# Kernel tuning notes

Measured on AMD Instinct MI355X. Metric: run time of the kernel, lower is better.

Reference implementation:

```python
import jax, jax.numpy as jnp
import numpy as np

B, N, D = 4, 2048, 1024
H, S, C, NSH, MV = 8, 3, 32, 3, 4


def _lin(key, fan_in, fan_out):
    k1, k2 = jax.random.split(key)
    lim = 1.0 / np.sqrt(fan_in)
    W = jax.random.uniform(k1, (fan_in, fan_out), minval=-lim, maxval=lim)
    b = jax.random.uniform(k2, (fan_out,), minval=-lim, maxval=lim)
    return W, b


def setup_inputs() -> dict:
    key = jax.random.key(0)
    ks = jax.random.split(key, 16)
    x = jax.random.normal(ks[0], (B, N, D), dtype=jnp.float32)
    W_sense, b_sense = _lin(ks[1], D, S * D)
    W_ctx, b_ctx = _lin(ks[2], D, D)
    W_sel, b_sel = _lin(ks[3], 2 * D, S)
    W_charge, b_charge = _lin(ks[4], D, 1)
    W_shell, b_shell = _lin(ks[5], D, NSH)
    W_class, b_class = _lin(ks[6], D, C)
    W_mass, b_mass = _lin(ks[7], D, 1)
    W_val, b_val = _lin(ks[8], D, MV)
    sparsity = 0.4
    init_val = -np.log(1.0 / sparsity - 1.0)
    compat_logits = jax.random.normal(ks[9], (C, C)) * 0.5 + init_val
    W_v, b_v = _lin(ks[10], D, D)
    W_out, b_out = _lin(ks[11], D, D)
    return {
        'x': x,
        'W_sense': W_sense, 'b_sense': b_sense,
        'W_ctx': W_ctx, 'b_ctx': b_ctx,
        'W_sel': W_sel, 'b_sel': b_sel,
        'W_charge': W_charge, 'b_charge': b_charge,
        'W_shell': W_shell, 'b_shell': b_shell,
        'W_class': W_class, 'b_class': b_class,
        'W_mass': W_mass, 'b_mass': b_mass,
        'W_val': W_val, 'b_val': b_val,
        'compat_logits': compat_logits.astype(jnp.float32),
        'w_charge': jnp.float32(1.0), 'w_shell': jnp.float32(0.5),
        'w_distance': jnp.float32(1.0), 'w_mass': jnp.float32(0.3),
        'w_valence': jnp.float32(0.3), 'temperature': jnp.float32(1.0),
        'W_v': W_v, 'b_v': b_v,
        'W_out': W_out, 'b_out': b_out,
    }


def reference(x, W_sense, b_sense, W_ctx, b_ctx, W_sel, b_sel,
              W_charge, b_charge, W_shell, b_shell, W_class, b_class,
              W_mass, b_mass, W_val, b_val, compat_logits,
              w_charge, w_shell, w_distance, w_mass, w_valence, temperature,
              W_v, b_v, W_out, b_out):
    b, n, d = x.shape
    sp = jax.nn.softplus

    # --- isotope selection (word-sense mixing) ---
    senses = (x @ W_sense + b_sense).reshape(b, n, S, d)          # (B,N,S,D)
    ctx_avg = (x @ W_ctx + b_ctx).mean(axis=1, keepdims=True)     # (B,1,D)
    sel_in = jnp.concatenate([x, jnp.broadcast_to(ctx_avg, (b, n, d))], axis=-1)
    sense_w = jax.nn.softmax(sel_in @ W_sel + b_sel, axis=-1)     # (B,N,S)
    x = jnp.einsum('bns,bnsd->bnd', sense_w, senses)

    # --- atomic properties ---
    charge = jnp.tanh(x @ W_charge + b_charge)[..., 0]            # (B,N)
    shell = jax.nn.softmax(x @ W_shell + b_shell, axis=-1)        # (B,N,NSH)
    cls = jnp.argmax(x @ W_class + b_class, axis=-1)              # (B,N) int
    mass = sp(x @ W_mass + b_mass)[..., 0] + 0.5                  # (B,N)
    val = jax.nn.softmax(x @ W_val + b_val, axis=-1)              # (B,N,MV)

    # --- class compatibility mask (B,N,N) ---
    compat = jax.nn.sigmoid((compat_logits + compat_logits.T) * 0.5)
    sparse_mask = compat[cls[:, :, None], cls[:, None, :]]

    # --- pairwise physics energy (B,N,N) ---
    pos = jnp.arange(n, dtype=x.dtype)
    dist = jnp.abs(pos[:, None] - pos[None, :])                   # (N,N)
    val_sum = val.sum(axis=-1)                                    # (B,N)
    E = (sp(w_charge) * charge[:, :, None] * charge[:, None, :]
         + sp(w_shell) * jnp.abs(shell[:, :, None, :] - shell[:, None, :, :]).sum(-1)
         - sp(w_distance) / (1.0 + 0.1 * dist)
         + sp(w_mass) * 0.1 * mass[:, :, None] * mass[:, None, :]
         - sp(w_valence) * (val_sum[:, :, None] + val_sum[:, None, :]) * 0.5)

    temp = sp(temperature)
    scores = (-E / temp) * sparse_mask
    causal = jnp.triu(jnp.ones((n, n), dtype=bool), k=1)
    scores = jnp.where(causal[None], -jnp.inf, scores)
    attn = jax.nn.softmax(scores, axis=-1)                        # (B,N,N)

    # --- weighted value aggregation (shared attn across heads) ---
    V = (x @ W_v + b_v).reshape(b, n, H, d // H)
    out = jnp.einsum('bij,bjhd->bihd', attn, V).reshape(b, n, d)
    return out @ W_out + b_out
```

## Files before the change

### kernel.cpp

```cpp
#include <hip/hip_runtime.h>
#include <hip/hip_bf16.h>
#include <cmath>

typedef __hip_bfloat16 bf16;
typedef __attribute__((ext_vector_type(4))) float floatx4;
typedef __attribute__((ext_vector_type(8))) short short8;
typedef __attribute__((ext_vector_type(8))) unsigned short ushort8;

__device__ __forceinline__ float bf2f(bf16 v) { return __bfloat162float(v); }
__device__ __forceinline__ bf16 f2bf(float v) { return __float2bfloat16(v); }
__device__ __forceinline__ float bfu2f(unsigned short u) { return __uint_as_float(((unsigned)u) << 16); }
__device__ __forceinline__ unsigned short f2bfu(float v) {
  bf16 h = __float2bfloat16(v);
  return __builtin_bit_cast(unsigned short, h);
}
__device__ __forceinline__ float softplusf(float x) {
  return x > 20.0f ? x : log1pf(expf(x));
}

__device__ __forceinline__ void async16(const void* g, void* l) {
  __builtin_amdgcn_global_load_lds(
      (const __attribute__((address_space(1))) unsigned int*)g,
      (__attribute__((address_space(3))) unsigned int*)l, 16, 0, 0);
}

template<int MODE, int CAUSAL, int ACCUM, int SWZ, int KSPLIT = 1>
__global__ __launch_bounds__(256, 3) void gemm_bt(
    const bf16* __restrict__ A, const bf16* __restrict__ Bt,
    const float* __restrict__ bias, void* __restrict__ Cptr,
    int M, int N, int K, int lda, int ldb, int ldc,
    long aoffz, long boffz, long coffz)
{
  __shared__ __align__(16) bf16 As[3][128 * 32];
  __shared__ __align__(16) bf16 Bs[3][128 * 32];

  const int tid = threadIdx.x;
  const int lane = tid & 63;
  const int wave = tid >> 6;
  const int wr = wave >> 1, wc = wave & 1;
  const long z = blockIdx.z;
  int kstart = 0;
  long zz = z;
  if (KSPLIT > 1) {
    kstart = (int)(z % KSPLIT) * K;
    zz = z / KSPLIT;
  }
  A += zz * aoffz;
  Bt += zz * boffz;

  int bx, by;
  if (SWZ) {
    const int mtiles = M >> 7;
    const int per = mtiles >> 3;
    const int bid = (int)blockIdx.x;
    const int xcd = bid & 7;
    const int slot = bid >> 3;
    by = xcd * per + (slot % per);
    bx = slot / per;
  } else {
    bx = blockIdx.x;
    by = blockIdx.y;
    if (CAUSAL) by = (int)gridDim.y - 1 - by;
  }
  const int m0 = by * 128, n0 = bx * 128;
  int kend = kstart + K;
  if (CAUSAL) {
    int klim = (by + 1) * 128;
    if (klim < kend) kend = klim;
  }

  const int ch0 = tid, ch1 = tid + 256;
  const int sw0 = ((ch0 & 3) ^ ((ch0 >> 3) & 3)) * 8;
  const int sw1 = ((ch1 & 3) ^ ((ch1 >> 3) & 3)) * 8;
  const size_t a0 = (size_t)(m0 + (ch0 >> 2)) * lda + sw0;
  const size_t a1 = (size_t)(m0 + (ch1 >> 2)) * lda + sw1;
  const size_t b0 = (size_t)(n0 + (ch0 >> 2)) * ldb + sw0;
  const size_t b1 = (size_t)(n0 + (ch1 >> 2)) * ldb + sw1;

  floatx4 acc[4][4] = {};
  const int fm = lane & 15, fq = lane >> 4;
  const int gph = (fm >> 1) & 3;
  const int nt = (kend - kstart) >> 5;

  auto stage = [&](int buf, int t) {
    const int k0 = kstart + t * 32;
    async16(&A[a0 + k0], &As[buf][ch0 * 8]);
    async16(&A[a1 + k0], &As[buf][ch1 * 8]);
    async16(&Bt[b0 + k0], &Bs[buf][ch0 * 8]);
    async16(&Bt[b1 + k0], &Bs[buf][ch1 * 8]);
  };

  stage(0, 0);
  if (nt > 1) {
    stage(1, 1);
    asm volatile("s_waitcnt vmcnt(4)" ::: "memory");
  } else {
    asm volatile("s_waitcnt vmcnt(0)" ::: "memory");
  }
  asm volatile("s_barrier" ::: "memory");

  int bufc = 0;
  for (int t = 0; t < nt; t++) {
    int bufn = bufc + 2; if (bufn >= 3) bufn -= 3;
    if (t + 2 < nt) stage(bufn, t + 2);
    short8 af[4], bfr[4];
#pragma unroll
    for (int i = 0; i < 4; i++) {
      int R = wr * 64 + i * 16 + fm;
      af[i] = *(const short8*)&As[bufc][R * 32 + ((fq ^ gph) << 3)];
    }
#pragma unroll
    for (int j = 0; j < 4; j++) {
      int R = wc * 64 + j * 16 + fm;
      bfr[j] = *(const short8*)&Bs[bufc][R * 32 + ((fq ^ gph) << 3)];
    }
#pragma unroll
    for (int i = 0; i < 4; i++)
#pragma unroll
      for (int j = 0; j < 4; j++)
        acc[i][j] = __builtin_amdgcn_mfma_f32_16x16x32_bf16(af[i], bfr[j], acc[i][j], 0, 0, 0);
    if (t + 2 < nt) asm volatile("s_waitcnt vmcnt(4)" ::: "memory");
    else            asm volatile("s_waitcnt vmcnt(0)" ::: "memory");
    asm volatile("s_barrier" ::: "memory");
    bufc++; if (bufc == 3) bufc = 0;
  }

  const int rm0 = (lane >> 4) * 4, cn = lane & 15;
#pragma unroll
  for (int i = 0; i < 4; i++) {
#pragma unroll
    for (int j = 0; j < 4; j++) {
      int nn = n0 + wc * 64 + j * 16 + cn;
      float bv = bias ? bias[nn] : 0.0f;
#pragma unroll
      for (int r = 0; r < 4; r++) {
        int mm = m0 + wr * 64 + i * 16 + rm0 + r;
        float v = acc[i][j][r] + bv;
        if (MODE == 0) {
          ((bf16*)Cptr)[z * coffz + (long)mm * ldc + nn] = f2bf(v);
        } else if (MODE == 1) {
          long idx = z * coffz + (long)mm * ldc + nn;
          float* Cf = (float*)Cptr;
          if (ACCUM) v += Cf[idx];
          Cf[idx] = v;
        } else {
          long idx = ((long)((mm >> 11) * 1024 + nn)) * 2048 + (mm & 2047);
          ((bf16*)Cptr)[idx] = f2bf(v);
        }
      }
    }
  }
}

__global__ __launch_bounds__(256, 3) void gemm_y(
    const bf16* __restrict__ A, const bf16* __restrict__ Bt,
    const float* __restrict__ bsense, const float* __restrict__ sw,
    bf16* __restrict__ y)
{
  __shared__ __align__(16) bf16 As[3][128 * 32];
  __shared__ __align__(16) bf16 Bs[3][128 * 32];

  const int tid = threadIdx.x;
  const int lane = tid & 63;
  const int wave = tid >> 6;
  const int wr = wave >> 1, wc = wave & 1;

  const int bid = (int)blockIdx.x;
  const int xcd = bid & 7;
  const int slot = bid >> 3;
  const int by = xcd * 8 + (slot & 7);
  const int bx = slot >> 3;
  const int m0 = by * 128, n0 = bx * 128;

  const int ch0 = tid, ch1 = tid + 256;
  const int sw0 = ((ch0 & 3) ^ ((ch0 >> 3) & 3)) * 8;
  const int sw1 = ((ch1 & 3) ^ ((ch1 >> 3) & 3)) * 8;
  const size_t a0 = (size_t)(m0 + (ch0 >> 2)) * 3072 + sw0;
  const size_t a1 = (size_t)(m0 + (ch1 >> 2)) * 3072 + sw1;
  const size_t b0 = (size_t)(n0 + (ch0 >> 2)) * 3072 + sw0;
  const size_t b1 = (size_t)(n0 + (ch1 >> 2)) * 3072 + sw1;

  floatx4 acc[4][4] = {};
  const int fm = lane & 15, fq = lane >> 4;
  const int gph = (fm >> 1) & 3;

  auto stage = [&](int buf, int t) {
    const int k0 = t * 32;
    async16(&A[a0 + k0], &As[buf][ch0 * 8]);
    async16(&A[a1 + k0], &As[buf][ch1 * 8]);
    async16(&Bt[b0 + k0], &Bs[buf][ch0 * 8]);
    async16(&Bt[b1 + k0], &Bs[buf][ch1 * 8]);
  };

  stage(0, 0);
  stage(1, 1);
  asm volatile("s_waitcnt vmcnt(4)" ::: "memory");
  asm volatile("s_barrier" ::: "memory");

  int bufc = 0;
  for (int t = 0; t < 96; t++) {
    int bufn = bufc + 2; if (bufn >= 3) bufn -= 3;
    if (t + 2 < 96) stage(bufn, t + 2);
    short8 af[4], bfr[4];
#pragma unroll
    for (int i = 0; i < 4; i++) {
      int R = wr * 64 + i * 16 + fm;
      af[i] = *(const short8*)&As[bufc][R * 32 + ((fq ^ gph) << 3)];
    }
#pragma unroll
    for (int j = 0; j < 4; j++) {
      int R = wc * 64 + j * 16 + fm;
      bfr[j] = *(const short8*)&Bs[bufc][R * 32 + ((fq ^ gph) << 3)];
    }
#pragma unroll
    for (int i = 0; i < 4; i++)
#pragma unroll
      for (int j = 0; j < 4; j++)
        acc[i][j] = __builtin_amdgcn_mfma_f32_16x16x32_bf16(af[i], bfr[j], acc[i][j], 0, 0, 0);
    if (t + 2 < 96) asm volatile("s_waitcnt vmcnt(4)" ::: "memory");
    else            asm volatile("s_waitcnt vmcnt(0)" ::: "memory");
    asm volatile("s_barrier" ::: "memory");
    bufc++; if (bufc == 3) bufc = 0;
  }

  const int rm0 = (lane >> 4) * 4, cn = lane & 15;
#pragma unroll
  for (int j = 0; j < 4; j++) {
    int nn = n0 + wc * 64 + j * 16 + cn;
    float bb0 = bsense[nn], bb1 = bsense[1024 + nn], bb2 = bsense[2048 + nn];
#pragma unroll
    for (int i = 0; i < 4; i++) {
#pragma unroll
      for (int r = 0; r < 4; r++) {
        int mm = m0 + wr * 64 + i * 16 + rm0 + r;
        const float* sm = sw + (size_t)mm * 4;
        float v = acc[i][j][r] + sm[0] * bb0 + sm[1] * bb1 + sm[2] * bb2;
        y[(size_t)mm * 1024 + nn] = f2bf(v);
      }
    }
  }
}

__global__ __launch_bounds__(256) void k_prescale(const float* __restrict__ x,
                                                  const float* __restrict__ sw,
                                                  bf16* __restrict__ Ap) {
  long id = (long)blockIdx.x * 256 + threadIdx.x;
  if (id >= 1048576L) return;
  int t = (int)(id >> 7);
  int kc = (int)(id & 127) << 3;
  const float* xt = x + (size_t)t * 1024 + kc;
  float4 a = *(const float4*)xt;
  float4 b = *(const float4*)(xt + 4);
  const float s0 = sw[t * 4 + 0], s1 = sw[t * 4 + 1], s2 = sw[t * 4 + 2];
  float v[8] = {a.x, a.y, a.z, a.w, b.x, b.y, b.z, b.w};
  ushort8 o0, o1, o2;
#pragma unroll
  for (int e = 0; e < 8; e++) {
    o0[e] = f2bfu(s0 * v[e]);
    o1[e] = f2bfu(s1 * v[e]);
    o2[e] = f2bfu(s2 * v[e]);
  }
  bf16* row = Ap + (size_t)t * 3072 + kc;
  *(ushort8*)(row) = o0;
  *(ushort8*)(row + 1024) = o1;
  *(ushort8*)(row + 2048) = o2;
}

__global__ __launch_bounds__(256) void k_split_x3(const float* __restrict__ x,
                                                  bf16* __restrict__ xhhl) {
  long id = (long)blockIdx.x * 256 + threadIdx.x;
  if (id >= 8388608L) return;
  long t = id >> 10;
  int d = (int)(id & 1023);
  float v = x[id];
  bf16 h = f2bf(v);
  bf16 l = f2bf(v - bf2f(h));
  bf16* row = xhhl + t * 3072;
  row[d] = h;
  row[1024 + d] = h;
  row[2048 + d] = l;
}

__global__ __launch_bounds__(256) void k_split_ws3(const float* __restrict__ Ws,
                                                   bf16* __restrict__ Wsn3) {
  long id = (long)blockIdx.x * 256 + threadIdx.x;
  if (id >= 3145728L) return;
  int row10 = (int)(id >> 10);
  int d = row10 / 3;
  int s = row10 - d * 3;
  int dp = (int)(id & 1023);
  float v = Ws[id];
  bf16 h = f2bf(v);
  bf16 l = f2bf(v - bf2f(h));
  bf16* row = Wsn3 + ((size_t)(s * 1024 + d)) * 3072;
  row[dp] = h;
  row[1024 + dp] = l;
  row[2048 + dp] = h;
}

__global__ __launch_bounds__(256) void k_trans_hl(const float* __restrict__ src,
                                                  bf16* __restrict__ dh,
                                                  int R, int C) {
  __shared__ float tile[32][33];
  int c0 = blockIdx.x * 32, r0 = blockIdx.y * 32;
  int tx = threadIdx.x & 31, ty = threadIdx.x >> 5;
  for (int rr = ty; rr < 32; rr += 8)
    tile[rr][tx] = src[(size_t)(r0 + rr) * C + c0 + tx];
  __syncthreads();
  for (int rr = ty; rr < 32; rr += 8)
    dh[(size_t)(c0 + rr) * R + r0 + tx] = f2bf(tile[tx][rr]);
}

__global__ __launch_bounds__(256) void k_trans_sense(const float* __restrict__ Ws,
                                                     bf16* __restrict__ Bt2) {
  __shared__ float tile[32][33];
  int c0 = blockIdx.x * 32, r0 = blockIdx.y * 32, s = blockIdx.z;
  int tx = threadIdx.x & 31, ty = threadIdx.x >> 5;
  for (int rr = ty; rr < 32; rr += 8)
    tile[rr][tx] = Ws[(size_t)(r0 + rr) * 3072 + s * 1024 + c0 + tx];
  __syncthreads();
  for (int rr = ty; rr < 32; rr += 8)
    Bt2[(size_t)(c0 + rr) * 3072 + s * 1024 + r0 + tx] = f2bf(tile[tx][rr]);
}

__global__ __launch_bounds__(256) void k_pack(
    const float* __restrict__ W_charge, const float* __restrict__ W_shell,
    const float* __restrict__ W_class, const float* __restrict__ W_mass,
    const float* __restrict__ b_charge, const float* __restrict__ b_shell,
    const float* __restrict__ b_class, const float* __restrict__ b_mass,
    const float* __restrict__ compat_logits,
    bf16* __restrict__ Whhl3, float* __restrict__ bhead, float* __restrict__ csig)
{
  int c = blockIdx.x;
  int tid = threadIdx.x;
  for (int e = tid; e < 1024; e += 256) {
    float v;
    if (c == 0) v = W_charge[e];
    else if (c < 4) v = W_shell[e * 3 + (c - 1)];
    else if (c == 4) v = W_mass[e];
    else if (c < 37) v = W_class[e * 32 + (c - 5)];
    else v = 0.0f;
    bf16 h = f2bf(v);
    bf16 l = f2bf(v - bf2f(h));
    bf16* row = Whhl3 + (size_t)c * 3072;
    row[e] = h;
    row[1024 + e] = h;
    row[2048 + e] = l;
  }
  if (c == 0 && tid < 37) {
    float v;
    if (tid == 0) v = b_charge[0];
    else if (tid < 4) v = b_shell[tid - 1];
    else if (tid == 4) v = b_mass[0];
    else v = b_class[tid - 5];
    bhead[tid] = v;
  }
  if (c == 1) {
    for (int k = tid; k < 1024; k += 256) {
      int ii = k >> 5, jj = k & 31;
      float l = 0.5f * (compat_logits[ii * 32 + jj] + compat_logits[jj * 32 + ii]);
      csig[k] = 1.0f / (1.0f + expf(-l));
    }
  }
}

__global__ __launch_bounds__(256) void k_bh(
    const float* __restrict__ b_sense, const float* __restrict__ W_charge,
    const float* __restrict__ W_shell, const float* __restrict__ W_class,
    const float* __restrict__ W_mass, float* __restrict__ bh)
{
  const int c = blockIdx.x, s = blockIdx.y;
  const int tid = threadIdx.x;
  __shared__ float red[256];
  float p = 0.0f;
  for (int e = tid; e < 1024; e += 256) {
    float w;
    if (c == 0) w = W_charge[e];
    else if (c < 4) w = W_shell[e * 3 + (c - 1)];
    else if (c == 4) w = W_mass[e];
    else w = W_class[e * 32 + (c - 5)];
    p += b_sense[s * 1024 + e] * w;
  }
  red[tid] = p;
  __syncthreads();
  for (int st = 128; st > 0; st >>= 1) {
    if (tid < st) red[tid] += red[tid + st];
    __syncthreads();
  }
  if (tid == 0) bh[s * 128 + c] = red[0];
}

__global__ __launch_bounds__(256) void k_reduce_mt(const float* __restrict__ Mtp,
                                                   float* __restrict__ Mt) {
  long o = (long)blockIdx.x * 256 + threadIdx.x;
  if (o >= 393216L) return;
  long s = o >> 17;
  long i = o & 131071;
  const float* p = Mtp + s * 8 * 131072 + i;
  float acc = 0.0f;
#pragma unroll
  for (int kc = 0; kc < 8; kc++) acc += p[(size_t)kc * 131072];
  Mt[o] = acc;
}

__global__ __launch_bounds__(256) void k_split(const float* __restrict__ Mt,
                                               const float* __restrict__ W_sel,
                                               bf16* __restrict__ Mthl) {
  long id = (long)blockIdx.x * 256 + threadIdx.x;
  if (id >= 1572864L) return;
  int n = (int)(id / 3072);
  int k = (int)(id - (long)n * 3072);
  int third = k >> 10;
  int j = k & 1023;
  float v;
  if (n < 384) {
    v = Mt[(size_t)n * 1024 + j];
  } else {
    int c2 = n - 384;
    v = (c2 < 3) ? W_sel[(size_t)j * 3 + c2] : 0.0f;
  }
  bf16 h = f2bf(v);
  Mthl[id] = (third == 1) ? f2bf(v - bf2f(h)) : h;
}

__global__ __launch_bounds__(256) void k_xbar(const float* __restrict__ x, float* __restrict__ xbar) {
  const int d = blockIdx.x * 256 + threadIdx.x;
  const int b = blockIdx.y;
  const int n0 = blockIdx.z * 256;
  const float* xb = x + (size_t)b * 2048 * 1024 + (size_t)n0 * 1024 + d;
  float s = 0.0f;
  for (int n = 0; n < 256; n++) s += xb[(size_t)n * 1024];
  atomicAdd(&xbar[b * 1024 + d], s * (1.0f / 2048.0f));
}

__global__ __launch_bounds__(256) void k_q(const float* __restrict__ W_ctx,
                                           const float* __restrict__ b_ctx,
                                           const float* __restrict__ W_sel,
                                           float* __restrict__ q) {
  const int e = blockIdx.x;
  const int tid = threadIdx.x;
  const float* row = (e < 1024) ? (W_ctx + (size_t)e * 1024) : b_ctx;
  float p0 = 0.0f, p1 = 0.0f, p2 = 0.0f;
  for (int d = tid; d < 1024; d += 256) {
    float v = row[d];
    const float* ws = W_sel + (size_t)(1024 + d) * 3;
    p0 += v * ws[0]; p1 += v * ws[1]; p2 += v * ws[2];
  }
  __shared__ float red[3][256];
  red[0][tid] = p0; red[1][tid] = p1; red[2][tid] = p2;
  __syncthreads();
  for (int st = 128; st > 0; st >>= 1) {
    if (tid < st) {
      red[0][tid] += red[0][tid + st];
      red[1][tid] += red[1][tid + st];
      red[2][tid] += red[2][tid + st];
    }
    __syncthreads();
  }
  if (tid < 3) q[(size_t)e * 3 + tid] = red[tid][0];
}

__global__ __launch_bounds__(256) void k_ctxsel(const float* __restrict__ xbar,
                                                const float* __restrict__ q,
                                                float* __restrict__ ctx_sel) {
  const int b = blockIdx.x;
  const int tid = threadIdx.x;
  float p0 = 0.0f, p1 = 0.0f, p2 = 0.0f;
  for (int e = tid; e < 1024; e += 256) {
    float v = xbar[b * 1024 + e];
    p0 += v * q[e * 3 + 0]; p1 += v * q[e * 3 + 1]; p2 += v * q[e * 3 + 2];
  }
  __shared__ float red[3][256];
  red[0][tid] = p0; red[1][tid] = p1; red[2][tid] = p2;
  __syncthreads();
  for (int st = 128; st > 0; st >>= 1) {
    if (tid < st) {
      red[0][tid] += red[0][tid + st];
      red[1][tid] += red[1][tid + st];
      red[2][tid] += red[2][tid + st];
    }
    __syncthreads();
  }
  if (tid < 3) ctx_sel[b * 3 + tid] = red[tid][0] + q[1024 * 3 + tid];
}

__global__ __launch_bounds__(64) void k_heads(
    const float* __restrict__ H, const float* __restrict__ ctx_sel,
    const float* __restrict__ b_sel, const float* __restrict__ bh,
    const float* __restrict__ bhead,
    float* __restrict__ sw, float* __restrict__ feat)
{
  const int t = blockIdx.x;
  const int b = t >> 11;
  const int lane = threadIdx.x;
  const float* Ht = H + (size_t)t * 512;
  const float* Ht2 = H + 4194304 + (size_t)t * 512;

  float s0 = Ht[384] + Ht2[384] + ctx_sel[b * 3 + 0] + b_sel[0];
  float s1 = Ht[385] + Ht2[385] + ctx_sel[b * 3 + 1] + b_sel[1];
  float s2 = Ht[386] + Ht2[386] + ctx_sel[b * 3 + 2] + b_sel[2];
  float mx = fmaxf(s0, fmaxf(s1, s2));
  float e0 = expf(s0 - mx), e1 = expf(s1 - mx), e2 = expf(s2 - mx);
  float inv = 1.0f / (e0 + e1 + e2);
  float w0 = e0 * inv, w1 = e1 * inv, w2 = e2 * inv;

  __shared__ float L[64];
  if (lane < 37) {
    float lg = bhead[lane];
    lg += w0 * (Ht[lane] + Ht2[lane] + bh[lane]);
    lg += w1 * (Ht[128 + lane] + Ht2[128 + lane] + bh[128 + lane]);
    lg += w2 * (Ht[256 + lane] + Ht2[256 + lane] + bh[256 + lane]);
    L[lane] = lg;
  }
  __syncthreads();
  if (lane == 0) {
    float charge = tanhf(L[0]);
    float h0 = L[1], h1 = L[2], h2 = L[3];
    float hm = fmaxf(h0, fmaxf(h1, h2));
    float x0 = expf(h0 - hm), x1 = expf(h1 - hm), x2 = expf(h2 - hm);
    float hinv = 1.0f / (x0 + x1 + x2);
    float mass = softplusf(L[4]) + 0.5f;
    int cls = 0;
    float best = L[5];
    for (int c = 1; c < 32; c++) {
      if (L[5 + c] > best) { best = L[5 + c]; cls = c; }
    }
    float* f = feat + (size_t)t * 8;
    f[0] = charge; f[1] = mass;
    f[2] = x0 * hinv; f[3] = x1 * hinv; f[4] = x2 * hinv;
    f[5] = (float)cls; f[6] = 0.0f; f[7] = 0.0f;
    float* sp_ = sw + (size_t)t * 4;
    sp_[0] = w0; sp_[1] = w1; sp_[2] = w2; sp_[3] = 0.0f;
  }
}

__global__ __launch_bounds__(256) void k_scores(
    const float* __restrict__ feat, const float* __restrict__ compat,
    const float* __restrict__ wchg, const float* __restrict__ wsh,
    const float* __restrict__ wdist, const float* __restrict__ wmass,
    const float* __restrict__ wval, const float* __restrict__ temp_p,
    bf16* __restrict__ P)
{
  const int i = blockIdx.x, b = blockIdx.y;
  const int tid = threadIdx.x;
  __shared__ float cs[1024];
  __shared__ float red[256];
  for (int k = tid; k < 1024; k += 256) cs[k] = compat[k];
  __syncthreads();

  const float a = softplusf(wchg[0]);
  const float bs = softplusf(wsh[0]);
  const float c = softplusf(wdist[0]);
  const float dm = softplusf(wmass[0]);
  const float ev = softplusf(wval[0]);
  const float itmp = 1.0f / softplusf(temp_p[0]);

  const float4* fi4 = (const float4*)(feat + ((size_t)b * 2048 + i) * 8);
  float4 fiA = fi4[0], fiB = fi4[1];
  const float ci = fiA.x, mi = fiA.y, si0 = fiA.z, si1 = fiA.w, si2 = fiB.x;
  int cli = (int)fiB.y; cli = cli < 0 ? 0 : (cli > 31 ? 31 : cli);

  float sc[8];
  float lmax = -3.0e38f;
#pragma unroll
  for (int jj = 0; jj < 8; jj++) {
    int j = tid + jj * 256;
    const float4* fj4 = (const float4*)(feat + ((size_t)b * 2048 + j) * 8);
    float4 fjA = fj4[0], fjB = fj4[1];
    int clj = (int)fjB.y; clj = clj < 0 ? 0 : (clj > 31 ? 31 : clj);
    float E = a * ci * fjA.x
            + bs * (fabsf(si0 - fjA.z) + fabsf(si1 - fjA.w) + fabsf(si2 - fjB.x))
            - c / (1.0f + 0.1f * fabsf((float)(i - j)))
            + dm * 0.1f * mi * fjA.y
            - ev;
    float s = (j <= i) ? (-E * itmp) * cs[cli * 32 + clj] : -3.0e38f;
    sc[jj] = s;
    lmax = fmaxf(lmax, s);
  }
  red[tid] = lmax;
  __syncthreads();
  for (int st = 128; st > 0; st >>= 1) {
    if (tid < st) red[tid] = fmaxf(red[tid], red[tid + st]);
    __syncthreads();
  }
  const float mrow = red[0];
  __syncthreads();

  float pv[8];
  float lsum = 0.0f;
#pragma unroll
  for (int jj = 0; jj < 8; jj++) {
    pv[jj] = (sc[jj] > -1.0e37f) ? expf(sc[jj] - mrow) : 0.0f;
    lsum += pv[jj];
  }
  red[tid] = lsum;
  __syncthreads();
  for (int st = 128; st > 0; st >>= 1) {
    if (tid < st) red[tid] += red[tid + st];
    __syncthreads();
  }
  const float inv = 1.0f / red[0];
  bf16* Pi = P + ((size_t)b * 2048 + i) * 2048;
#pragma unroll
  for (int jj = 0; jj < 8; jj++) Pi[tid + jj * 256] = f2bf(pv[jj] * inv);
}

extern "C" void kernel_launch(void* const* d_in, const int* in_sizes, int n_in,
                              void* d_out, int out_size, void* d_ws, size_t ws_size,
                              hipStream_t stream) {
  (void)in_sizes; (void)n_in; (void)out_size; (void)ws_size;
  const float* x        = (const float*)d_in[0];
  const float* W_sense  = (const float*)d_in[1];
  const float* b_sense  = (const float*)d_in[2];
  const float* W_ctx    = (const float*)d_in[3];
  const float* b_ctx    = (const float*)d_in[4];
  const float* W_sel    = (const float*)d_in[5];
  const float* b_sel    = (const float*)d_in[6];
  const float* W_charge = (const float*)d_in[7];
  const float* b_charge = (const float*)d_in[8];
  const float* W_shell  = (const float*)d_in[9];
  const float* b_shell  = (const float*)d_in[10];
  const float* W_class  = (const float*)d_in[11];
  const float* b_class  = (const float*)d_in[12];
  const float* W_mass   = (const float*)d_in[13];
  const float* b_mass   = (const float*)d_in[14];
  const float* compat_logits = (const float*)d_in[17];
  const float* w_charge = (const float*)d_in[18];
  const float* w_shell  = (const float*)d_in[19];
  const float* w_distance = (const float*)d_in[20];
  const float* w_mass   = (const float*)d_in[21];
  const float* w_valence = (const float*)d_in[22];
  const float* temperature = (const float*)d_in[23];
  const float* W_v      = (const float*)d_in[24];
  const float* b_v      = (const float*)d_in[25];
  const float* W_out    = (const float*)d_in[26];
  const float* b_out    = (const float*)d_in[27];

  char* w = (char*)d_ws;
  auto alloc = [&](size_t bytes) {
    char* p = w;
    w += (bytes + 255) & ~(size_t)255;
    return p;
  };
  bf16* xhhl  = (bf16*)alloc(8192ULL * 3072 * 2);
  char* R1    = alloc(48ULL * 1024 * 1024);
  bf16* Wsn3  = (bf16*)R1;
  float* Hh   = (float*)R1;
  float* Mtp  = (float*)(R1 + 20ULL * 1024 * 1024);
  bf16* Mthl  = (bf16*)(R1 + 40ULL * 1024 * 1024);
  float* Mt   = (float*)(R1 + 44ULL * 1024 * 1024);
  bf16* y     = (bf16*)R1;
  bf16* Wts2  = (bf16*)alloc(3072ULL * 1024 * 2);
  bf16* Wt_v  = (bf16*)alloc(1024ULL * 1024 * 2);
  bf16* Wt_out = (bf16*)alloc(1024ULL * 1024 * 2);
  bf16* Whhl3 = (bf16*)alloc(128ULL * 3072 * 2);
  float* bh   = (float*)alloc(3ULL * 128 * 4);
  float* bhead = (float*)alloc(256);
  float* csig = (float*)alloc(4096);
  float* xbar = (float*)alloc(4ULL * 1024 * 4);
  float* qbuf = (float*)alloc(1025ULL * 3 * 4);
  float* ctx_sel = (float*)alloc(256);
  float* feat = (float*)alloc(8192ULL * 8 * 4);
  float* sw   = (float*)alloc(8192ULL * 4 * 4);
  bf16* Aprime = xhhl;
  bf16* Vt = xhhl + 8388608;
  bf16* O  = xhhl + 16777216;
  bf16* P  = (bf16*)d_out;

  k_split_x3<<<32768, 256, 0, stream>>>(x, xhhl);
  k_split_ws3<<<12288, 256, 0, stream>>>(W_sense, Wsn3);
  k_trans_sense<<<dim3(32, 32, 3), 256, 0, stream>>>(W_sense, Wts2);
  k_trans_hl<<<dim3(32, 32), 256, 0, stream>>>(W_v, Wt_v, 1024, 1024);
  k_trans_hl<<<dim3(32, 32), 256, 0, stream>>>(W_out, Wt_out, 1024, 1024);
  k_pack<<<128, 256, 0, stream>>>(W_charge, W_shell, W_class, W_mass,
                                  b_charge, b_shell, b_class, b_mass,
                                  compat_logits, Whhl3, bhead, csig);

  hipMemsetAsync(xbar, 0, 4096 * 4, stream);
  k_xbar<<<dim3(4, 4, 8), 256, 0, stream>>>(x, xbar);
  k_q<<<1025, 256, 0, stream>>>(W_ctx, b_ctx, W_sel, qbuf);
  k_ctxsel<<<4, 256, 0, stream>>>(xbar, qbuf, ctx_sel);

  gemm_bt<1, 0, 0, 0, 8><<<dim3(8, 1, 24), 256, 0, stream>>>(
      Whhl3, Wsn3, nullptr, Mtp, 128, 1024, 384, 3072, 3072, 1024,
      0, 3145728L, 131072L);
  k_reduce_mt<<<1536, 256, 0, stream>>>(Mtp, Mt);
  k_split<<<6144, 256, 0, stream>>>(Mt, W_sel, Mthl);

  gemm_bt<1, 0, 0, 1, 2><<<dim3(256, 1, 2), 256, 0, stream>>>(
      xhhl, Mthl, nullptr, Hh, 8192, 512, 1536, 3072, 3072, 512,
      0, 0, 4194304L);

  k_bh<<<dim3(37, 3), 256, 0, stream>>>(b_sense, W_charge, W_shell, W_class, W_mass, bh);
  k_heads<<<8192, 64, 0, stream>>>(Hh, ctx_sel, b_sel, bh, bhead, sw, feat);

  k_prescale<<<4096, 256, 0, stream>>>(x, sw, Aprime);

  gemm_y<<<512, 256, 0, stream>>>(Aprime, Wts2, b_sense, sw, y);

  gemm_bt<2, 0, 0, 1><<<512, 256, 0, stream>>>(
      y, Wt_v, b_v, Vt, 8192, 1024, 1024, 1024, 1024, 0, 0, 0, 0);

  k_scores<<<dim3(2048, 4), 256, 0, stream>>>(feat, csig, w_charge, w_shell,
                                              w_distance, w_mass, w_valence, temperature, P);

  gemm_bt<0, 1, 0, 0><<<dim3(8, 16, 4), 256, 0, stream>>>(
      P, Vt, nullptr, O, 2048, 1024, 2048, 2048, 2048, 1024,
      2048L * 2048, 1024L * 2048, 2048L * 1024);

  gemm_bt<1, 0, 0, 1><<<512, 256, 0, stream>>>(
      O, Wt_out, b_out, (float*)d_out, 8192, 1024, 1024, 1024, 1024, 1024, 0, 0, 0);
}
```

Before: 542.4 us.

## Use 8-wave 512-thread GEMM blocks and pack four tokens per k_heads block

The GEMM kernels move from 256 to 512 threads per 128x128 tile. Each of the 8 waves now computes a 32x64 sub-tile, and each thread issues one async load per operand per stage instead of two, with the vmcnt waits adjusted to match. The aim is more waves per tile for latency hiding and lower per-wave register pressure, at the cost of less fragment reuse per wave and more barrier participants. k_heads is also changed to process four tokens per 256-thread block, cutting block count and launch overhead.

```diff
diff --git a/kernel.cpp b/kernel.cpp
--- a/kernel.cpp
+++ b/kernel.cpp
@@ -25,7 +25,7 @@
 }
 
 template<int MODE, int CAUSAL, int ACCUM, int SWZ, int KSPLIT = 1>
-__global__ __launch_bounds__(256, 3) void gemm_bt(
+__global__ __launch_bounds__(512, 4) void gemm_bt(
     const bf16* __restrict__ A, const bf16* __restrict__ Bt,
     const float* __restrict__ bias, void* __restrict__ Cptr,
     int M, int N, int K, int lda, int ldb, int ldc,
@@ -69,31 +69,26 @@
     if (klim < kend) kend = klim;
   }
 
-  const int ch0 = tid, ch1 = tid + 256;
-  const int sw0 = ((ch0 & 3) ^ ((ch0 >> 3) & 3)) * 8;
-  const int sw1 = ((ch1 & 3) ^ ((ch1 >> 3) & 3)) * 8;
-  const size_t a0 = (size_t)(m0 + (ch0 >> 2)) * lda + sw0;
-  const size_t a1 = (size_t)(m0 + (ch1 >> 2)) * lda + sw1;
-  const size_t b0 = (size_t)(n0 + (ch0 >> 2)) * ldb + sw0;
-  const size_t b1 = (size_t)(n0 + (ch1 >> 2)) * ldb + sw1;
-
-  floatx4 acc[4][4] = {};
+  const int srow = tid >> 2, sc = tid & 3;
+  const int scol = (sc ^ ((srow >> 1) & 3)) * 8;
+  const size_t a0 = (size_t)(m0 + srow) * lda + scol;
+  const size_t b0 = (size_t)(n0 + srow) * ldb + scol;
+
+  floatx4 acc[2][4] = {};
   const int fm = lane & 15, fq = lane >> 4;
   const int gph = (fm >> 1) & 3;
   const int nt = (kend - kstart) >> 5;
 
   auto stage = [&](int buf, int t) {
     const int k0 = kstart + t * 32;
-    async16(&A[a0 + k0], &As[buf][ch0 * 8]);
-    async16(&A[a1 + k0], &As[buf][ch1 * 8]);
-    async16(&Bt[b0 + k0], &Bs[buf][ch0 * 8]);
-    async16(&Bt[b1 + k0], &Bs[buf][ch1 * 8]);
+    async16(&A[a0 + k0], &As[buf][tid * 8]);
+    async16(&Bt[b0 + k0], &Bs[buf][tid * 8]);
   };
 
   stage(0, 0);
   if (nt > 1) {
     stage(1, 1);
-    asm volatile("s_waitcnt vmcnt(4)" ::: "memory");
+    asm volatile("s_waitcnt vmcnt(2)" ::: "memory");
   } else {
     asm volatile("s_waitcnt vmcnt(0)" ::: "memory");
   }
@@ -103,10 +98,10 @@
   for (int t = 0; t < nt; t++) {
     int bufn = bufc + 2; if (bufn >= 3) bufn -= 3;
     if (t + 2 < nt) stage(bufn, t + 2);
-    short8 af[4], bfr[4];
-#pragma unroll
-    for (int i = 0; i < 4; i++) {
-      int R = wr * 64 + i * 16 + fm;
+    short8 af[2], bfr[4];
+#pragma unroll
+    for (int i = 0; i < 2; i++) {
+      int R = wr * 32 + i * 16 + fm;
       af[i] = *(const short8*)&As[bufc][R * 32 + ((fq ^ gph) << 3)];
     }
 #pragma unroll
@@ -115,11 +110,11 @@
       bfr[j] = *(const short8*)&Bs[bufc][R * 32 + ((fq ^ gph) << 3)];
     }
 #pragma unroll
-    for (int i = 0; i < 4; i++)
+    for (int i = 0; i < 2; i++)
 #pragma unroll
       for (int j = 0; j < 4; j++)
         acc[i][j] = __builtin_amdgcn_mfma_f32_16x16x32_bf16(af[i], bfr[j], acc[i][j], 0, 0, 0);
-    if (t + 2 < nt) asm volatile("s_waitcnt vmcnt(4)" ::: "memory");
+    if (t + 2 < nt) asm volatile("s_waitcnt vmcnt(2)" ::: "memory");
     else            asm volatile("s_waitcnt vmcnt(0)" ::: "memory");
     asm volatile("s_barrier" ::: "memory");
     bufc++; if (bufc == 3) bufc = 0;
@@ -127,14 +122,14 @@
 
   const int rm0 = (lane >> 4) * 4, cn = lane & 15;
 #pragma unroll
-  for (int i = 0; i < 4; i++) {
+  for (int i = 0; i < 2; i++) {
 #pragma unroll
     for (int j = 0; j < 4; j++) {
       int nn = n0 + wc * 64 + j * 16 + cn;
       float bv = bias ? bias[nn] : 0.0f;
 #pragma unroll
       for (int r = 0; r < 4; r++) {
-        int mm = m0 + wr * 64 + i * 16 + rm0 + r;
+        int mm = m0 + wr * 32 + i * 16 + rm0 + r;
         float v = acc[i][j][r] + bv;
         if (MODE == 0) {
           ((bf16*)Cptr)[z * coffz + (long)mm * ldc + nn] = f2bf(v);
@@ -152,7 +147,7 @@
   }
 }
 
-__global__ __launch_bounds__(256, 3) void gemm_y(
+__global__ __launch_bounds__(512, 4) void gemm_y(
     const bf16* __restrict__ A, const bf16* __restrict__ Bt,
     const float* __restrict__ bsense, const float* __restrict__ sw,
     bf16* __restrict__ y)
@@ -172,39 +167,34 @@
   const int bx = slot >> 3;
   const int m0 = by * 128, n0 = bx * 128;
 
-  const int ch0 = tid, ch1 = tid + 256;
-  const int sw0 = ((ch0 & 3) ^ ((ch0 >> 3) & 3)) * 8;
-  const int sw1 = ((ch1 & 3) ^ ((ch1 >> 3) & 3)) * 8;
-  const size_t a0 = (size_t)(m0 + (ch0 >> 2)) * 3072 + sw0;
-  const size_t a1 = (size_t)(m0 + (ch1 >> 2)) * 3072 + sw1;
-  const size_t b0 = (size_t)(n0 + (ch0 >> 2)) * 3072 + sw0;
-  const size_t b1 = (size_t)(n0 + (ch1 >> 2)) * 3072 + sw1;
-
-  floatx4 acc[4][4] = {};
+  const int srow = tid >> 2, sc = tid & 3;
+  const int scol = (sc ^ ((srow >> 1) & 3)) * 8;
+  const size_t a0 = (size_t)(m0 + srow) * 3072 + scol;
+  const size_t b0 = (size_t)(n0 + srow) * 3072 + scol;
+
+  floatx4 acc[2][4] = {};
   const int fm = lane & 15, fq = lane >> 4;
   const int gph = (fm >> 1) & 3;
 
   auto stage = [&](int buf, int t) {
     const int k0 = t * 32;
-    async16(&A[a0 + k0], &As[buf][ch0 * 8]);
-    async16(&A[a1 + k0], &As[buf][ch1 * 8]);
-    async16(&Bt[b0 + k0], &Bs[buf][ch0 * 8]);
-    async16(&Bt[b1 + k0], &Bs[buf][ch1 * 8]);
+    async16(&A[a0 + k0], &As[buf][tid * 8]);
+    async16(&Bt[b0 + k0], &Bs[buf][tid * 8]);
   };
 
   stage(0, 0);
   stage(1, 1);
-  asm volatile("s_waitcnt vmcnt(4)" ::: "memory");
+  asm volatile("s_waitcnt vmcnt(2)" ::: "memory");
   asm volatile("s_barrier" ::: "memory");
 
   int bufc = 0;
   for (int t = 0; t < 96; t++) {
     int bufn = bufc + 2; if (bufn >= 3) bufn -= 3;
     if (t + 2 < 96) stage(bufn, t + 2);
-    short8 af[4], bfr[4];
-#pragma unroll
-    for (int i = 0; i < 4; i++) {
-      int R = wr * 64 + i * 16 + fm;
+    short8 af[2], bfr[4];
+#pragma unroll
+    for (int i = 0; i < 2; i++) {
+      int R = wr * 32 + i * 16 + fm;
       af[i] = *(const short8*)&As[bufc][R * 32 + ((fq ^ gph) << 3)];
     }
 #pragma unroll
@@ -213,11 +203,11 @@
       bfr[j] = *(const short8*)&Bs[bufc][R * 32 + ((fq ^ gph) << 3)];
     }
 #pragma unroll
-    for (int i = 0; i < 4; i++)
+    for (int i = 0; i < 2; i++)
 #pragma unroll
       for (int j = 0; j < 4; j++)
         acc[i][j] = __builtin_amdgcn_mfma_f32_16x16x32_bf16(af[i], bfr[j], acc[i][j], 0, 0, 0);
-    if (t + 2 < 96) asm volatile("s_waitcnt vmcnt(4)" ::: "memory");
+    if (t + 2 < 96) asm volatile("s_waitcnt vmcnt(2)" ::: "memory");
     else            asm volatile("s_waitcnt vmcnt(0)" ::: "memory");
     asm volatile("s_barrier" ::: "memory");
     bufc++; if (bufc == 3) bufc = 0;
@@ -229,10 +219,10 @@
     int nn = n0 + wc * 64 + j * 16 + cn;
     float bb0 = bsense[nn], bb1 = bsense[1024 + nn], bb2 = bsense[2048 + nn];
 #pragma unroll
-    for (int i = 0; i < 4; i++) {
+    for (int i = 0; i < 2; i++) {
 #pragma unroll
       for (int r = 0; r < 4; r++) {
-        int mm = m0 + wr * 64 + i * 16 + rm0 + r;
+        int mm = m0 + wr * 32 + i * 16 + rm0 + r;
         const float* sm = sw + (size_t)mm * 4;
         float v = acc[i][j][r] + sm[0] * bb0 + sm[1] * bb1 + sm[2] * bb2;
         y[(size_t)mm * 1024 + nn] = f2bf(v);
@@ -484,15 +474,16 @@
   if (tid < 3) ctx_sel[b * 3 + tid] = red[tid][0] + q[1024 * 3 + tid];
 }
 
-__global__ __launch_bounds__(64) void k_heads(
+__global__ __launch_bounds__(256) void k_heads(
     const float* __restrict__ H, const float* __restrict__ ctx_sel,
     const float* __restrict__ b_sel, const float* __restrict__ bh,
     const float* __restrict__ bhead,
     float* __restrict__ sw, float* __restrict__ feat)
 {
-  const int t = blockIdx.x;
+  const int g = threadIdx.x >> 6;
+  const int lane = threadIdx.x & 63;
+  const int t = blockIdx.x * 4 + g;
   const int b = t >> 11;
-  const int lane = threadIdx.x;
   const float* Ht = H + (size_t)t * 512;
   const float* Ht2 = H + 4194304 + (size_t)t * 512;
 
@@ -504,26 +495,26 @@
   float inv = 1.0f / (e0 + e1 + e2);
   float w0 = e0 * inv, w1 = e1 * inv, w2 = e2 * inv;
 
-  __shared__ float L[64];
+  __shared__ float L[4][64];
   if (lane < 37) {
     float lg = bhead[lane];
     lg += w0 * (Ht[lane] + Ht2[lane] + bh[lane]);
     lg += w1 * (Ht[128 + lane] + Ht2[128 + lane] + bh[128 + lane]);
     lg += w2 * (Ht[256 + lane] + Ht2[256 + lane] + bh[256 + lane]);
-    L[lane] = lg;
+    L[g][lane] = lg;
   }
   __syncthreads();
   if (lane == 0) {
-    float charge = tanhf(L[0]);
-    float h0 = L[1], h1 = L[2], h2 = L[3];
+    float charge = tanhf(L[g][0]);
+    float h0 = L[g][1], h1 = L[g][2], h2 = L[g][3];
     float hm = fmaxf(h0, fmaxf(h1, h2));
     float x0 = expf(h0 - hm), x1 = expf(h1 - hm), x2 = expf(h2 - hm);
     float hinv = 1.0f / (x0 + x1 + x2);
-    float mass = softplusf(L[4]) + 0.5f;
+    float mass = softplusf(L[g][4]) + 0.5f;
     int cls = 0;
-    float best = L[5];
+    float best = L[g][5];
     for (int c = 1; c < 32; c++) {
-      if (L[5 + c] > best) { best = L[5 + c]; cls = c; }
+      if (L[g][5 + c] > best) { best = L[g][5 + c]; cls = c; }
     }
     float* f = feat + (size_t)t * 8;
     f[0] = charge; f[1] = mass;
@@ -681,33 +672,33 @@
   k_q<<<1025, 256, 0, stream>>>(W_ctx, b_ctx, W_sel, qbuf);
   k_ctxsel<<<4, 256, 0, stream>>>(xbar, qbuf, ctx_sel);
 
-  gemm_bt<1, 0, 0, 0, 8><<<dim3(8, 1, 24), 256, 0, stream>>>(
+  gemm_bt<1, 0, 0, 0, 8><<<dim3(8, 1, 24), 512, 0, stream>>>(
       Whhl3, Wsn3, nullptr, Mtp, 128, 1024, 384, 3072, 3072, 1024,
       0, 3145728L, 131072L);
   k_reduce_mt<<<1536, 256, 0, stream>>>(Mtp, Mt);
   k_split<<<6144, 256, 0, stream>>>(Mt, W_sel, Mthl);
 
-  gemm_bt<1, 0, 0, 1, 2><<<dim3(256, 1, 2), 256, 0, stream>>>(
+  gemm_bt<1, 0, 0, 1, 2><<<dim3(256, 1, 2), 512, 0, stream>>>(
       xhhl, Mthl, nullptr, Hh, 8192, 512, 1536, 3072, 3072, 512,
       0, 0, 4194304L);
 
   k_bh<<<dim3(37, 3), 256, 0, stream>>>(b_sense, W_charge, W_shell, W_class, W_mass, bh);
-  k_heads<<<8192, 64, 0, stream>>>(Hh, ctx_sel, b_sel, bh, bhead, sw, feat);
+  k_heads<<<2048, 256, 0, stream>>>(Hh, ctx_sel, b_sel, bh, bhead, sw, feat);
 
   k_prescale<<<4096, 256, 0, stream>>>(x, sw, Aprime);
 
-  gemm_y<<<512, 256, 0, stream>>>(Aprime, Wts2, b_sense, sw, y);
-
-  gemm_bt<2, 0, 0, 1><<<512, 256, 0, stream>>>(
+  gemm_y<<<512, 512, 0, stream>>>(Aprime, Wts2, b_sense, sw, y);
+
+  gemm_bt<2, 0, 0, 1><<<512, 512, 0, stream>>>(
       y, Wt_v, b_v, Vt, 8192, 1024, 1024, 1024, 1024, 0, 0, 0, 0);
 
   k_scores<<<dim3(2048, 4), 256, 0, stream>>>(feat, csig, w_charge, w_shell,
                                               w_distance, w_mass, w_valence, temperature, P);
 
-  gemm_bt<0, 1, 0, 0><<<dim3(8, 16, 4), 256, 0, stream>>>(
+  gemm_bt<0, 1, 0, 0><<<dim3(8, 16, 4), 512, 0, stream>>>(
       P, Vt, nullptr, O, 2048, 1024, 2048, 2048, 2048, 1024,
       2048L * 2048, 1024L * 2048, 2048L * 1024);
 
-  gemm_bt<1, 0, 0, 1><<<512, 256, 0, stream>>>(
+  gemm_bt<1, 0, 0, 1><<<512, 512, 0, stream>>>(
       O, Wt_out, b_out, (float*)d_out, 8192, 1024, 1024, 1024, 1024, 1024, 0, 0, 0);
 }
```

Result: faster. 515.7 us (-4.9%).
